# Kernel optimization log

Hardware: AMD Instinct MI355X
Metric: run time of the kernel (lower is better)

The kernel has to match this reference:

```python
import jax, jax.numpy as jnp
import numpy as np

H, T, D = 16, 2048, 1024
DH = D // H  # 64


def setup_inputs() -> dict:
    key = jax.random.key(0)
    ks = jax.random.split(key, 6)
    state = jax.random.normal(ks[0], (H, DH, DH), jnp.float32) * 0.02  # per-head recurrent state
    x = jax.random.normal(ks[1], (T, D), jnp.float32)
    done = jax.random.uniform(ks[2], (T,)) < (4.0 / T)  # sparse episode-reset flags (bool)
    w_qkv = jax.random.normal(ks[3], (D, 3 * D), jnp.float32) / np.sqrt(D)
    b_qkv = jnp.zeros((3 * D,), jnp.float32)
    w_out = jax.random.normal(ks[4], (D, D), jnp.float32) / np.sqrt(D)
    b_out = jnp.zeros((D,), jnp.float32)
    return {"state": state, "x": x, "done": done, "w_qkv": w_qkv,
            "b_qkv": b_qkv, "w_out": w_out, "b_out": b_out}


def _mha_forward(state, x, done, w_qkv, b_qkv, w_out, b_out):
    # qkv projection; einops 'T (QKV H Dh) -> QKV H T Dh'
    qkv = (x @ w_qkv + b_qkv).reshape(T, 3, H, DH).transpose(1, 2, 0, 3)
    q, k, v = qkv[0], qkv[1], qkv[2]  # each (H, T, Dh)

    cum = jnp.cumsum(done.astype(jnp.int32))  # inclusive cumsum, as in done.cumsum()
    before_first = cum == 0            # tokens before first reset (attend to carried state)
    after_last = cum == cum[-1]        # tokens after last reset (feed new state)
    done_any = cum[-1] > 0

    # make_attn_mask(done): causal AND no reset index i with s < i <= t.
    # The scanned mask equals: causal & (cum[t] == cum[s]) (same-segment).
    t_idx = jnp.arange(T)
    mask = (t_idx[:, None] >= t_idx[None, :]) & (cum[:, None] == cum[None, :])  # (T, T)

    attn = jnp.where(mask[None], jnp.einsum('htd,hsd->hts', q, k), 0.0)  # mask * (q @ k.T)
    q_bef = q * before_first[None, :, None]
    out = jnp.einsum('hts,hsd->htd', attn, v) + jnp.einsum('htd,hde->hte', q_bef, state)

    k_aft = k * after_last[None, :, None]
    v_aft = v * after_last[None, :, None]
    s_new = jnp.einsum('htd,hte->hde', k_aft, v_aft)  # k_aft.T @ v_aft per head
    new_state = jnp.where(done_any, s_new, state + s_new)

    # 'H T Dh -> T (H Dh)' then output projection
    x_out = out.transpose(1, 0, 2).reshape(T, D) @ w_out + b_out
    return new_state, x_out


def reference(state, x, done, w_qkv, b_qkv, w_out, b_out):
    return _mha_forward(state, x, done, w_qkv, b_qkv, w_out, b_out)
```

## Files before the change

### kernel.cpp

```cpp
#include <hip/hip_runtime.h>

#define TT 2048
#define DD 1024
#define HH 16
#define DH 64
#define QKV_N 3072
#define QKW 2048

typedef __attribute__((ext_vector_type(8))) short bf16x8;
typedef __attribute__((ext_vector_type(4))) short short4v;
typedef __attribute__((ext_vector_type(4))) float f32x4;

__device__ inline short f2bf(float f) {
    union { float f; unsigned u; } v; v.f = f;
    unsigned r = v.u + 0x7fff + ((v.u >> 16) & 1);
    return (short)(r >> 16);
}

__device__ inline f32x4 mfma16(bf16x8 a, bf16x8 b, f32x4 c) {
    return __builtin_amdgcn_mfma_f32_16x16x32_bf16(a, b, c, 0, 0, 0);
}

__device__ __forceinline__ void gload16(const void* g, void* l) {
    __builtin_amdgcn_global_load_lds(
        (const __attribute__((address_space(1))) unsigned int*)g,
        (__attribute__((address_space(3))) unsigned int*)l, 16, 0, 0);
}

__global__ __launch_bounds__(256) void scan_kernel(const int* __restrict__ done,
                                                   int* __restrict__ seg,
                                                   int* __restrict__ totalp,
                                                   int* __restrict__ aux) {
    __shared__ int part[256];
    __shared__ int excl[256];
    __shared__ int segl[2048];
    __shared__ int tot;
    int tid = threadIdx.x;
    int base = tid * 8;
    int local[8];
    int run = 0;
#pragma unroll
    for (int i = 0; i < 8; ++i) { run += (done[base + i] != 0) ? 1 : 0; local[i] = run; }
    part[tid] = run;
    __syncthreads();
    if (tid < 64) {
        int p4[4];
#pragma unroll
        for (int i = 0; i < 4; ++i) p4[i] = part[tid * 4 + i];
        int s = p4[0] + p4[1] + p4[2] + p4[3];
        int v = s;
#pragma unroll
        for (int off = 1; off < 64; off <<= 1) {
            int u = __shfl_up(v, off);
            if (tid >= off) v += u;
        }
        int ex = v - s;
#pragma unroll
        for (int i = 0; i < 4; ++i) { excl[tid * 4 + i] = ex; ex += p4[i]; }
        if (tid == 63) { totalp[0] = v; tot = v; }
    }
    __syncthreads();
    int off = excl[tid];
#pragma unroll
    for (int i = 0; i < 8; ++i) {
        int sv = off + local[i];
        seg[base + i] = sv;
        segl[base + i] = sv;
    }
    __syncthreads();
    if (tid < 33) {
        int target = (tid < 32) ? segl[tid * 64] : tot;
        int lo = 0, hi = 2047;
        while (lo < hi) { int mid = (lo + hi) >> 1; if (segl[mid] >= target) hi = mid; else lo = mid + 1; }
        aux[tid] = lo >> 6;
    }
}

__device__ void transpose_tile(const float* __restrict__ in, short* __restrict__ out,
                               int R, int C, int r0, int c0, float (*tile)[65]) {
    int tid = threadIdx.x;
#pragma unroll
    for (int p = 0; p < 4; ++p) {
        int ch = tid + p * 256;
        int r = ch >> 4, c4 = (ch & 15) * 4;
        float4 v = *(const float4*)&in[(size_t)(r0 + r) * C + c0 + c4];
        tile[r][c4] = v.x; tile[r][c4 + 1] = v.y; tile[r][c4 + 2] = v.z; tile[r][c4 + 3] = v.w;
    }
    __syncthreads();
#pragma unroll
    for (int p = 0; p < 2; ++p) {
        int ch = tid + p * 256;
        int c = ch >> 3, r8 = (ch & 7) * 8;
        short tmp[8];
#pragma unroll
        for (int i = 0; i < 8; ++i) tmp[i] = f2bf(tile[r8 + i][c]);
        *(float4*)&out[(size_t)(c0 + c) * R + r0 + r8] = *(float4*)tmp;
    }
}

__global__ __launch_bounds__(256) void prep_kernel(const float* __restrict__ x,
                                                   const float* __restrict__ w_qkv,
                                                   const float* __restrict__ w_out,
                                                   const float* __restrict__ state,
                                                   const int* __restrict__ totalp,
                                                   short* __restrict__ x_bf,
                                                   short* __restrict__ wqT,
                                                   short* __restrict__ woT,
                                                   short* __restrict__ stT,
                                                   float* __restrict__ stout) {
    __shared__ float tile[64][65];
    int b = blockIdx.x;
    if (b < 1024) {
        int i = (b * 256 + threadIdx.x) * 8;
        float4 a = *(const float4*)&x[i];
        float4 c = *(const float4*)&x[i + 4];
        short tmp[8] = {f2bf(a.x), f2bf(a.y), f2bf(a.z), f2bf(a.w),
                        f2bf(c.x), f2bf(c.y), f2bf(c.z), f2bf(c.w)};
        *(float4*)&x_bf[i] = *(float4*)tmp;
    } else if (b < 1792) {
        int bb = b - 1024;
        transpose_tile(w_qkv, wqT, DD, QKV_N, (bb & 15) * 64, (bb >> 4) * 64, tile);
    } else if (b < 2048) {
        int bb = b - 1792;
        transpose_tile(w_out, woT, DD, DD, (bb & 15) * 64, (bb >> 4) * 64, tile);
    } else if (b < 2064) {
        int h = b - 2048;
        transpose_tile(state + (size_t)h * 4096, stT + (size_t)h * 4096, DH, DH, 0, 0, tile);
    } else {
        int f = ((b - 2064) * 256 + threadIdx.x) * 4;
        bool done_any = totalp[0] > 0;
        float4 v = done_any ? make_float4(0.f, 0.f, 0.f, 0.f) : *(const float4*)&state[f];
        *(float4*)&stout[f] = v;
    }
}

__global__ __launch_bounds__(256) void gemm_qkv(const short* __restrict__ A,
                                                const short* __restrict__ BT,
                                                const float* __restrict__ bias,
                                                short* __restrict__ qk,
                                                short* __restrict__ vt) {
    __shared__ short As[128 * 32];
    __shared__ short Bs[128 * 32];
    const int K = DD, N = QKV_N;
    int tid = threadIdx.x;
    int wave = tid >> 6, lane = tid & 63;
    int quad = lane >> 4, l15 = lane & 15;
    int m0 = blockIdx.x * 128, n0 = blockIdx.y * 128;
    int wr = (wave >> 1) * 64, wc = (wave & 1) * 64;

    int srow = wave * 16 + (lane >> 2);
    int scol = (lane & 3) * 8;
    const short* Ag = A + (size_t)(m0 + srow) * K + scol;
    const short* Bg = BT + (size_t)(n0 + srow) * K + scol;
    short* As0 = &As[(wave * 16) * 32];
    short* As1 = &As[(64 + wave * 16) * 32];
    short* Bs0 = &Bs[(wave * 16) * 32];
    short* Bs1 = &Bs[(64 + wave * 16) * 32];

    f32x4 acc[4][4] = {};
    for (int k0 = 0; k0 < K; k0 += 32) {
        __syncthreads();
        gload16(Ag + k0, As0);
        gload16(Ag + (size_t)64 * K + k0, As1);
        gload16(Bg + k0, Bs0);
        gload16(Bg + (size_t)64 * K + k0, Bs1);
        __syncthreads();
        bf16x8 af[4], bfr[4];
#pragma unroll
        for (int i = 0; i < 4; ++i) {
            af[i]  = *(const bf16x8*)&As[(wr + i * 16 + l15) * 32 + quad * 8];
            bfr[i] = *(const bf16x8*)&Bs[(wc + i * 16 + l15) * 32 + quad * 8];
        }
#pragma unroll
        for (int i = 0; i < 4; ++i)
#pragma unroll
            for (int j = 0; j < 4; ++j)
                acc[i][j] = mfma16(af[i], bfr[j], acc[i][j]);
    }

    if (n0 < 2048) {
#pragma unroll
        for (int i = 0; i < 4; ++i)
#pragma unroll
            for (int j = 0; j < 4; ++j)
#pragma unroll
                for (int r = 0; r < 4; ++r) {
                    int row = m0 + wr + i * 16 + quad * 4 + r;
                    int col = n0 + wc + j * 16 + l15;
                    qk[(size_t)row * QKW + col] = f2bf(acc[i][j][r] + bias[col]);
                }
    } else {
#pragma unroll
        for (int j = 0; j < 4; ++j) {
            int col = n0 + wc + j * 16 + l15;
            float bv = bias[col];
            int eg = col - 2048;
            int hh = eg >> 6, e = eg & 63;
#pragma unroll
            for (int i = 0; i < 4; ++i) {
                int tb = m0 + wr + i * 16 + quad * 4;
                short4v pk;
#pragma unroll
                for (int r = 0; r < 4; ++r) pk[r] = f2bf(acc[i][j][r] + bv);
                *(short4v*)&vt[(size_t)hh * (DH * TT) + (size_t)e * TT + tb] = pk;
            }
        }
    }
}

__global__ __launch_bounds__(256) void attn_mfma(const short* __restrict__ qk,
                                                 const short* __restrict__ vt,
                                                 const short* __restrict__ stT,
                                                 const int* __restrict__ seg,
                                                 const int* __restrict__ aux,
                                                 short* __restrict__ outb) {
    __shared__ short Ss_lo[64 * 32];
    __shared__ short Ss_hi[64 * 32];

    int h = blockIdx.x, tt = blockIdx.y;
    int t0 = tt * 64;
    int tid = threadIdx.x, wave = tid >> 6, lane = tid & 63;
    int quad = lane >> 4, l15 = lane & 15;
    int myt = wave * 16;

    const short* qrow = qk + (size_t)(t0 + myt + l15) * QKW + h * DH + quad * 8;
    bf16x8 qf0 = *(const bf16x8*)qrow;
    bf16x8 qf1 = *(const bf16x8*)(qrow + 32);

    int tlane = t0 + myt + l15;
    int seg_lane = seg[tlane];
    int segt_r[4];
#pragma unroll
    for (int r = 0; r < 4; ++r) segt_r[r] = seg[t0 + myt + quad * 4 + r];

    f32x4 accT[4] = {};
    if (seg[t0] == 0) {
        const short* sb = stT + (size_t)h * 4096;
#pragma unroll
        for (int j = 0; j < 4; ++j) {
            const short* srow = sb + (j * 16 + l15) * 64 + quad * 8;
            bf16x8 a0 = *(const bf16x8*)srow;
            bf16x8 a1 = *(const bf16x8*)(srow + 32);
            accT[j] = mfma16(a0, qf0, accT[j]);
            accT[j] = mfma16(a1, qf1, accT[j]);
        }
        if (seg_lane != 0) {
#pragma unroll
            for (int j = 0; j < 4; ++j)
#pragma unroll
                for (int r = 0; r < 4; ++r) accT[j][r] = 0.f;
        }
    }

    short* ss_lo = &Ss_lo[myt * 32];
    short* ss_hi = &Ss_hi[myt * 32];
    const short* kbase = qk + 1024 + h * DH;
    const short* vbase = vt + (size_t)h * (DH * TT);

    int st0 = aux[tt];
    for (int st = st0; st <= tt; ++st) {
        int s0 = st * 64;
        f32x4 sacc[4] = {};
#pragma unroll
        for (int j = 0; j < 4; ++j) {
            const short* krow = kbase + (size_t)(s0 + j * 16 + l15) * QKW + quad * 8;
            bf16x8 b0 = *(const bf16x8*)krow;
            bf16x8 b1 = *(const bf16x8*)(krow + 32);
            sacc[j] = mfma16(qf0, b0, sacc[j]);
            sacc[j] = mfma16(qf1, b1, sacc[j]);
        }
        bool last = (st == tt);
#pragma unroll
        for (int j = 0; j < 4; ++j) {
            int sgl = s0 + j * 16 + l15;
            int seg_s = seg[sgl];
#pragma unroll
            for (int r = 0; r < 4; ++r) {
                bool ok = (seg_s == segt_r[r]);
                if (last) ok = ok && (sgl <= t0 + myt + quad * 4 + r);
                short v = ok ? f2bf(sacc[j][r]) : (short)0;
                int row = quad * 4 + r;
                if (j < 2) ss_lo[row * 32 + j * 16 + l15] = v;
                else       ss_hi[row * 32 + (j - 2) * 16 + l15] = v;
            }
        }
        bf16x8 sf0 = *(const bf16x8*)&ss_lo[l15 * 32 + quad * 8];
        bf16x8 sf1 = *(const bf16x8*)&ss_hi[l15 * 32 + quad * 8];
#pragma unroll
        for (int j = 0; j < 4; ++j) {
            const short* vrow = vbase + (size_t)(j * 16 + l15) * TT + s0 + quad * 8;
            bf16x8 a0 = *(const bf16x8*)vrow;
            bf16x8 a1 = *(const bf16x8*)(vrow + 32);
            accT[j] = mfma16(a0, sf0, accT[j]);
            accT[j] = mfma16(a1, sf1, accT[j]);
        }
    }

#pragma unroll
    for (int j = 0; j < 4; ++j) {
        short4v pk;
#pragma unroll
        for (int r = 0; r < 4; ++r) pk[r] = f2bf(accT[j][r]);
        *(short4v*)&outb[(size_t)tlane * DD + h * DH + j * 16 + quad * 4] = pk;
    }
}

__global__ __launch_bounds__(256) void state_mfma(const short* __restrict__ qk,
                                                  const short* __restrict__ vt,
                                                  const int* __restrict__ seg,
                                                  const int* __restrict__ totalp,
                                                  const int* __restrict__ aux,
                                                  float* __restrict__ out) {
    __shared__ short Kt_lo[64 * 32];
    __shared__ short Kt_hi[64 * 32];
    int h = blockIdx.x, ct = blockIdx.y;
    if (ct < aux[32]) return;
    int t0 = ct * 64;
    int total = totalp[0];
    int tid = threadIdx.x, wave = tid >> 6, lane = tid & 63;
    int quad = lane >> 4, l15 = lane & 15;
    int myd = wave * 16;

    {
        bool keep = (seg[t0 + lane] == total);
        const short* src = qk + (size_t)(t0 + lane) * QKW + 1024 + h * DH + myd;
        union { float4 f; short s[8]; } u0, u1;
        u0.f = keep ? *(const float4*)src : make_float4(0.f, 0.f, 0.f, 0.f);
        u1.f = keep ? *(const float4*)(src + 8) : make_float4(0.f, 0.f, 0.f, 0.f);
        short* dst = (lane < 32) ? &Kt_lo[lane] : &Kt_hi[lane - 32];
#pragma unroll
        for (int i = 0; i < 8; ++i) {
            dst[(myd + i) * 32] = u0.s[i];
            dst[(myd + 8 + i) * 32] = u1.s[i];
        }
    }
    bf16x8 a0 = *(const bf16x8*)&Kt_lo[(myd + l15) * 32 + quad * 8];
    bf16x8 a1 = *(const bf16x8*)&Kt_hi[(myd + l15) * 32 + quad * 8];

    const short* vbase = vt + (size_t)h * (DH * TT);
    f32x4 acc[4] = {};
#pragma unroll
    for (int j = 0; j < 4; ++j) {
        const short* vrow = vbase + (size_t)(j * 16 + l15) * TT + t0 + quad * 8;
        bf16x8 b0 = *(const bf16x8*)vrow;
        bf16x8 b1 = *(const bf16x8*)(vrow + 32);
        acc[j] = mfma16(a0, b0, acc[j]);
        acc[j] = mfma16(a1, b1, acc[j]);
    }
    float* oh = out + (size_t)h * 4096;
#pragma unroll
    for (int j = 0; j < 4; ++j)
#pragma unroll
        for (int r = 0; r < 4; ++r)
            atomicAdd(&oh[(myd + quad * 4 + r) * DH + j * 16 + l15], acc[j][r]);
}

__global__ __launch_bounds__(256) void gemm_out(const short* __restrict__ A,
                                                const short* __restrict__ BT,
                                                const float* __restrict__ bias,
                                                float* __restrict__ Cout,
                                                int M, int N, int K) {
    __shared__ short As[128 * 32];
    __shared__ short Bs[128 * 32];
    int tid = threadIdx.x;
    int wave = tid >> 6, lane = tid & 63;
    int quad = lane >> 4, l15 = lane & 15;
    int m0 = blockIdx.x * 128, n0 = blockIdx.y * 128;
    int wr = (wave >> 1) * 64, wc = (wave & 1) * 64;

    int srow = wave * 16 + (lane >> 2);
    int scol = (lane & 3) * 8;
    const short* Ag = A + (size_t)(m0 + srow) * K + scol;
    const short* Bg = BT + (size_t)(n0 + srow) * K + scol;
    short* As0 = &As[(wave * 16) * 32];
    short* As1 = &As[(64 + wave * 16) * 32];
    short* Bs0 = &Bs[(wave * 16) * 32];
    short* Bs1 = &Bs[(64 + wave * 16) * 32];

    f32x4 acc[4][4] = {};
    for (int k0 = 0; k0 < K; k0 += 32) {
        __syncthreads();
        gload16(Ag + k0, As0);
        gload16(Ag + (size_t)64 * K + k0, As1);
        gload16(Bg + k0, Bs0);
        gload16(Bg + (size_t)64 * K + k0, Bs1);
        __syncthreads();
        bf16x8 af[4], bfr[4];
#pragma unroll
        for (int i = 0; i < 4; ++i) {
            af[i]  = *(const bf16x8*)&As[(wr + i * 16 + l15) * 32 + quad * 8];
            bfr[i] = *(const bf16x8*)&Bs[(wc + i * 16 + l15) * 32 + quad * 8];
        }
#pragma unroll
        for (int i = 0; i < 4; ++i)
#pragma unroll
            for (int j = 0; j < 4; ++j)
                acc[i][j] = mfma16(af[i], bfr[j], acc[i][j]);
    }
#pragma unroll
    for (int i = 0; i < 4; ++i)
#pragma unroll
        for (int j = 0; j < 4; ++j)
#pragma unroll
            for (int r = 0; r < 4; ++r) {
                int row = m0 + wr + i * 16 + quad * 4 + r;
                int col = n0 + wc + j * 16 + l15;
                Cout[(size_t)row * N + col] = acc[i][j][r] + bias[col];
            }
}

extern "C" void kernel_launch(void* const* d_in, const int* in_sizes, int n_in,
                              void* d_out, int out_size, void* d_ws, size_t ws_size,
                              hipStream_t stream) {
    const float* state = (const float*)d_in[0];
    const float* x     = (const float*)d_in[1];
    const int*   done  = (const int*)d_in[2];
    const float* w_qkv = (const float*)d_in[3];
    const float* b_qkv = (const float*)d_in[4];
    const float* w_out = (const float*)d_in[5];
    const float* b_out = (const float*)d_in[6];

    char* ws = (char*)d_ws;
    int*   seg    = (int*)ws;
    int*   totalp = (int*)(ws + 8192);
    int*   aux    = (int*)(ws + 8256);
    short* wqT    = (short*)(ws + 8448);
    short* woT    = (short*)(ws + 6299904);
    short* stT    = (short*)(ws + 8397056);
    short* qk     = (short*)(ws + 8528128);
    short* vt     = (short*)(ws + 16916736);
    short* xbf_outb = (short*)(ws + 21111040);

    float* new_state_out = (float*)d_out;
    float* x_out         = (float*)d_out + HH * DH * DH;

    scan_kernel<<<1, 256, 0, stream>>>(done, seg, totalp, aux);
    prep_kernel<<<2128, 256, 0, stream>>>(x, w_qkv, w_out, state, totalp,
                                          xbf_outb, wqT, woT, stT, new_state_out);

    gemm_qkv<<<dim3(TT / 128, QKV_N / 128), 256, 0, stream>>>(
        xbf_outb, wqT, b_qkv, qk, vt);

    attn_mfma<<<dim3(HH, TT / 64), 256, 0, stream>>>(qk, vt, stT, seg, aux, xbf_outb);

    state_mfma<<<dim3(HH, TT / 64), 256, 0, stream>>>(qk, vt, seg, totalp, aux,
                                                      new_state_out);

    gemm_out<<<dim3(TT / 128, DD / 128), 256, 0, stream>>>(
        xbf_outb, woT, b_out, x_out, TT, DD, DD);
}
```

Measured before the change: 183.0 us.

## Split attention key range across chunks, fuse scan into prep and state into attention

The standalone scan kernel is folded into an extra block of the prep kernel, and the done_any check for the state copy is recomputed locally from the done flags. The state-update kernel becomes a fifth z-slice of the attention launch. Attention for each query tile is split across up to four key-chunk groups of eight tiles, with partial fp32 results written to a workspace and summed by a new reduce kernel. K and V loads are hoisted ahead of the MFMAs in each key-tile iteration. This aims to cut launch count and the serial load imbalance of long segments, at the cost of extra partial-sum traffic and one more kernel launch.

```diff
diff --git a/kernel.cpp b/kernel.cpp
--- a/kernel.cpp
+++ b/kernel.cpp
@@ -27,55 +27,6 @@
         (__attribute__((address_space(3))) unsigned int*)l, 16, 0, 0);
 }
 
-__global__ __launch_bounds__(256) void scan_kernel(const int* __restrict__ done,
-                                                   int* __restrict__ seg,
-                                                   int* __restrict__ totalp,
-                                                   int* __restrict__ aux) {
-    __shared__ int part[256];
-    __shared__ int excl[256];
-    __shared__ int segl[2048];
-    __shared__ int tot;
-    int tid = threadIdx.x;
-    int base = tid * 8;
-    int local[8];
-    int run = 0;
-#pragma unroll
-    for (int i = 0; i < 8; ++i) { run += (done[base + i] != 0) ? 1 : 0; local[i] = run; }
-    part[tid] = run;
-    __syncthreads();
-    if (tid < 64) {
-        int p4[4];
-#pragma unroll
-        for (int i = 0; i < 4; ++i) p4[i] = part[tid * 4 + i];
-        int s = p4[0] + p4[1] + p4[2] + p4[3];
-        int v = s;
-#pragma unroll
-        for (int off = 1; off < 64; off <<= 1) {
-            int u = __shfl_up(v, off);
-            if (tid >= off) v += u;
-        }
-        int ex = v - s;
-#pragma unroll
-        for (int i = 0; i < 4; ++i) { excl[tid * 4 + i] = ex; ex += p4[i]; }
-        if (tid == 63) { totalp[0] = v; tot = v; }
-    }
-    __syncthreads();
-    int off = excl[tid];
-#pragma unroll
-    for (int i = 0; i < 8; ++i) {
-        int sv = off + local[i];
-        seg[base + i] = sv;
-        segl[base + i] = sv;
-    }
-    __syncthreads();
-    if (tid < 33) {
-        int target = (tid < 32) ? segl[tid * 64] : tot;
-        int lo = 0, hi = 2047;
-        while (lo < hi) { int mid = (lo + hi) >> 1; if (segl[mid] >= target) hi = mid; else lo = mid + 1; }
-        aux[tid] = lo >> 6;
-    }
-}
-
 __device__ void transpose_tile(const float* __restrict__ in, short* __restrict__ out,
                                int R, int C, int r0, int c0, float (*tile)[65]) {
     int tid = threadIdx.x;
@@ -102,16 +53,21 @@
                                                    const float* __restrict__ w_qkv,
                                                    const float* __restrict__ w_out,
                                                    const float* __restrict__ state,
-                                                   const int* __restrict__ totalp,
+                                                   const int* __restrict__ done,
                                                    short* __restrict__ x_bf,
                                                    short* __restrict__ wqT,
                                                    short* __restrict__ woT,
                                                    short* __restrict__ stT,
-                                                   float* __restrict__ stout) {
+                                                   float* __restrict__ stout,
+                                                   int* __restrict__ seg,
+                                                   int* __restrict__ totalp,
+                                                   int* __restrict__ aux) {
     __shared__ float tile[64][65];
+    __shared__ int scanbuf[2048 + 512 + 1];
     int b = blockIdx.x;
+    int tid = threadIdx.x;
     if (b < 1024) {
-        int i = (b * 256 + threadIdx.x) * 8;
+        int i = (b * 256 + tid) * 8;
         float4 a = *(const float4*)&x[i];
         float4 c = *(const float4*)&x[i + 4];
         short tmp[8] = {f2bf(a.x), f2bf(a.y), f2bf(a.z), f2bf(a.w),
@@ -126,11 +82,60 @@
     } else if (b < 2064) {
         int h = b - 2048;
         transpose_tile(state + (size_t)h * 4096, stT + (size_t)h * 4096, DH, DH, 0, 0, tile);
+    } else if (b < 2128) {
+        __shared__ int anyf;
+        if (tid == 0) anyf = 0;
+        __syncthreads();
+        int acc = 0;
+#pragma unroll
+        for (int i = 0; i < 8; ++i) acc |= done[tid * 8 + i];
+        if (acc) anyf = 1;
+        __syncthreads();
+        int f = ((b - 2064) * 256 + tid) * 4;
+        float4 v = anyf ? make_float4(0.f, 0.f, 0.f, 0.f) : *(const float4*)&state[f];
+        *(float4*)&stout[f] = v;
     } else {
-        int f = ((b - 2064) * 256 + threadIdx.x) * 4;
-        bool done_any = totalp[0] > 0;
-        float4 v = done_any ? make_float4(0.f, 0.f, 0.f, 0.f) : *(const float4*)&state[f];
-        *(float4*)&stout[f] = v;
+        int* segl = scanbuf;
+        int* part = scanbuf + 2048;
+        int* excl = scanbuf + 2304;
+        int base = tid * 8;
+        int local[8];
+        int run = 0;
+#pragma unroll
+        for (int i = 0; i < 8; ++i) { run += (done[base + i] != 0) ? 1 : 0; local[i] = run; }
+        part[tid] = run;
+        __syncthreads();
+        if (tid < 64) {
+            int p4[4];
+#pragma unroll
+            for (int i = 0; i < 4; ++i) p4[i] = part[tid * 4 + i];
+            int s = p4[0] + p4[1] + p4[2] + p4[3];
+            int v = s;
+#pragma unroll
+            for (int off = 1; off < 64; off <<= 1) {
+                int u = __shfl_up(v, off);
+                if (tid >= off) v += u;
+            }
+            int ex = v - s;
+#pragma unroll
+            for (int i = 0; i < 4; ++i) { excl[tid * 4 + i] = ex; ex += p4[i]; }
+            if (tid == 63) { totalp[0] = v; scanbuf[2560] = v; }
+        }
+        __syncthreads();
+        int off = excl[tid];
+#pragma unroll
+        for (int i = 0; i < 8; ++i) {
+            int sv = off + local[i];
+            seg[base + i] = sv;
+            segl[base + i] = sv;
+        }
+        __syncthreads();
+        if (tid < 33) {
+            int target = (tid < 32) ? segl[tid * 64] : scanbuf[2560];
+            int lo = 0, hi = 2047;
+            while (lo < hi) { int mid = (lo + hi) >> 1; if (segl[mid] >= target) hi = mid; else lo = mid + 1; }
+            aux[tid] = lo >> 6;
+        }
     }
 }
 
@@ -141,7 +146,7 @@
                                                 short* __restrict__ vt) {
     __shared__ short As[128 * 32];
     __shared__ short Bs[128 * 32];
-    const int K = DD, N = QKV_N;
+    const int K = DD;
     int tid = threadIdx.x;
     int wave = tid >> 6, lane = tid & 63;
     int quad = lane >> 4, l15 = lane & 15;
@@ -212,16 +217,64 @@
                                                  const short* __restrict__ vt,
                                                  const short* __restrict__ stT,
                                                  const int* __restrict__ seg,
+                                                 const int* __restrict__ totalp,
                                                  const int* __restrict__ aux,
-                                                 short* __restrict__ outb) {
+                                                 short* __restrict__ outb,
+                                                 float* __restrict__ part,
+                                                 float* __restrict__ nsout) {
     __shared__ short Ss_lo[64 * 32];
     __shared__ short Ss_hi[64 * 32];
 
-    int h = blockIdx.x, tt = blockIdx.y;
+    int h = blockIdx.x, tt = blockIdx.y, sc = blockIdx.z;
     int t0 = tt * 64;
     int tid = threadIdx.x, wave = tid >> 6, lane = tid & 63;
     int quad = lane >> 4, l15 = lane & 15;
     int myt = wave * 16;
+    const short* vbase = vt + (size_t)h * (DH * TT);
+
+    if (sc == 4) {
+        if (tt < aux[32]) return;
+        int total = totalp[0];
+        int myd = myt;
+        {
+            bool keep = (seg[t0 + lane] == total);
+            const short* src = qk + (size_t)(t0 + lane) * QKW + 1024 + h * DH + myd;
+            union { float4 f; short s[8]; } u0, u1;
+            u0.f = keep ? *(const float4*)src : make_float4(0.f, 0.f, 0.f, 0.f);
+            u1.f = keep ? *(const float4*)(src + 8) : make_float4(0.f, 0.f, 0.f, 0.f);
+            short* dst = (lane < 32) ? &Ss_lo[lane] : &Ss_hi[lane - 32];
+#pragma unroll
+            for (int i = 0; i < 8; ++i) {
+                dst[(myd + i) * 32] = u0.s[i];
+                dst[(myd + 8 + i) * 32] = u1.s[i];
+            }
+        }
+        bf16x8 a0 = *(const bf16x8*)&Ss_lo[(myd + l15) * 32 + quad * 8];
+        bf16x8 a1 = *(const bf16x8*)&Ss_hi[(myd + l15) * 32 + quad * 8];
+        f32x4 acc[4] = {};
+#pragma unroll
+        for (int j = 0; j < 4; ++j) {
+            const short* vrow = vbase + (size_t)(j * 16 + l15) * TT + t0 + quad * 8;
+            bf16x8 b0 = *(const bf16x8*)vrow;
+            bf16x8 b1 = *(const bf16x8*)(vrow + 32);
+            acc[j] = mfma16(a0, b0, acc[j]);
+            acc[j] = mfma16(a1, b1, acc[j]);
+        }
+        float* oh = nsout + (size_t)h * 4096;
+#pragma unroll
+        for (int j = 0; j < 4; ++j)
+#pragma unroll
+            for (int r = 0; r < 4; ++r)
+                atomicAdd(&oh[(myd + quad * 4 + r) * DH + j * 16 + l15], acc[j][r]);
+        return;
+    }
+
+    int st0 = aux[tt];
+    int sc_lo = st0 >> 3, sc_hi = tt >> 3;
+    if (sc < sc_lo || sc > sc_hi) return;
+    bool direct = (sc_lo == sc_hi);
+    int st_lo = (st0 > sc * 8) ? st0 : sc * 8;
+    int st_hi = (tt < sc * 8 + 7) ? tt : sc * 8 + 7;
 
     const short* qrow = qk + (size_t)(t0 + myt + l15) * QKW + h * DH + quad * 8;
     bf16x8 qf0 = *(const bf16x8*)qrow;
@@ -234,7 +287,7 @@
     for (int r = 0; r < 4; ++r) segt_r[r] = seg[t0 + myt + quad * 4 + r];
 
     f32x4 accT[4] = {};
-    if (seg[t0] == 0) {
+    if (sc == sc_lo && seg[t0] == 0) {
         const short* sb = stT + (size_t)h * 4096;
 #pragma unroll
         for (int j = 0; j < 4; ++j) {
@@ -255,28 +308,39 @@
     short* ss_lo = &Ss_lo[myt * 32];
     short* ss_hi = &Ss_hi[myt * 32];
     const short* kbase = qk + 1024 + h * DH;
-    const short* vbase = vt + (size_t)h * (DH * TT);
-
-    int st0 = aux[tt];
-    for (int st = st0; st <= tt; ++st) {
+
+    for (int st = st_lo; st <= st_hi; ++st) {
         int s0 = st * 64;
+        int segv[4];
+#pragma unroll
+        for (int j = 0; j < 4; ++j) segv[j] = seg[s0 + j * 16 + l15];
+        bf16x8 kb0[4], kb1[4];
+#pragma unroll
+        for (int j = 0; j < 4; ++j) {
+            const short* krow = kbase + (size_t)(s0 + j * 16 + l15) * QKW + quad * 8;
+            kb0[j] = *(const bf16x8*)krow;
+            kb1[j] = *(const bf16x8*)(krow + 32);
+        }
+        bf16x8 va0[4], va1[4];
+#pragma unroll
+        for (int j = 0; j < 4; ++j) {
+            const short* vrow = vbase + (size_t)(j * 16 + l15) * TT + s0 + quad * 8;
+            va0[j] = *(const bf16x8*)vrow;
+            va1[j] = *(const bf16x8*)(vrow + 32);
+        }
         f32x4 sacc[4] = {};
 #pragma unroll
         for (int j = 0; j < 4; ++j) {
-            const short* krow = kbase + (size_t)(s0 + j * 16 + l15) * QKW + quad * 8;
-            bf16x8 b0 = *(const bf16x8*)krow;
-            bf16x8 b1 = *(const bf16x8*)(krow + 32);
-            sacc[j] = mfma16(qf0, b0, sacc[j]);
-            sacc[j] = mfma16(qf1, b1, sacc[j]);
+            sacc[j] = mfma16(qf0, kb0[j], sacc[j]);
+            sacc[j] = mfma16(qf1, kb1[j], sacc[j]);
         }
         bool last = (st == tt);
 #pragma unroll
         for (int j = 0; j < 4; ++j) {
             int sgl = s0 + j * 16 + l15;
-            int seg_s = seg[sgl];
 #pragma unroll
             for (int r = 0; r < 4; ++r) {
-                bool ok = (seg_s == segt_r[r]);
+                bool ok = (segv[j] == segt_r[r]);
                 if (last) ok = ok && (sgl <= t0 + myt + quad * 4 + r);
                 short v = ok ? f2bf(sacc[j][r]) : (short)0;
                 int row = quad * 4 + r;
@@ -288,71 +352,49 @@
         bf16x8 sf1 = *(const bf16x8*)&ss_hi[l15 * 32 + quad * 8];
 #pragma unroll
         for (int j = 0; j < 4; ++j) {
-            const short* vrow = vbase + (size_t)(j * 16 + l15) * TT + s0 + quad * 8;
-            bf16x8 a0 = *(const bf16x8*)vrow;
-            bf16x8 a1 = *(const bf16x8*)(vrow + 32);
-            accT[j] = mfma16(a0, sf0, accT[j]);
-            accT[j] = mfma16(a1, sf1, accT[j]);
-        }
-    }
-
-#pragma unroll
-    for (int j = 0; j < 4; ++j) {
+            accT[j] = mfma16(va0[j], sf0, accT[j]);
+            accT[j] = mfma16(va1[j], sf1, accT[j]);
+        }
+    }
+
+    if (direct) {
+#pragma unroll
+        for (int j = 0; j < 4; ++j) {
+            short4v pk;
+#pragma unroll
+            for (int r = 0; r < 4; ++r) pk[r] = f2bf(accT[j][r]);
+            *(short4v*)&outb[(size_t)tlane * DD + h * DH + j * 16 + quad * 4] = pk;
+        }
+    } else {
+        float* pb = part + (((size_t)(h * 32 + tt) * 4 + sc) * 4096);
+#pragma unroll
+        for (int j = 0; j < 4; ++j)
+            *(f32x4*)&pb[(myt + l15) * 64 + j * 16 + quad * 4] = accT[j];
+    }
+}
+
+__global__ __launch_bounds__(256) void attn_reduce(const float* __restrict__ part,
+                                                   const int* __restrict__ aux,
+                                                   short* __restrict__ outb) {
+    int h = blockIdx.x, tt = blockIdx.y;
+    int sc_lo = aux[tt] >> 3, sc_hi = tt >> 3;
+    if (sc_lo == sc_hi) return;
+    int t0 = tt * 64;
+    int tid = threadIdx.x;
+    int tl16 = tid >> 4, e4 = (tid & 15) * 4;
+    const float* pb = part + ((size_t)(h * 32 + tt) * 4) * 4096;
+#pragma unroll
+    for (int p = 0; p < 4; ++p) {
+        int tl = p * 16 + tl16;
+        float4 acc = make_float4(0.f, 0.f, 0.f, 0.f);
+        for (int sc = sc_lo; sc <= sc_hi; ++sc) {
+            float4 v = *(const float4*)&pb[sc * 4096 + tl * 64 + e4];
+            acc.x += v.x; acc.y += v.y; acc.z += v.z; acc.w += v.w;
+        }
         short4v pk;
-#pragma unroll
-        for (int r = 0; r < 4; ++r) pk[r] = f2bf(accT[j][r]);
-        *(short4v*)&outb[(size_t)tlane * DD + h * DH + j * 16 + quad * 4] = pk;
-    }
-}
-
-__global__ __launch_bounds__(256) void state_mfma(const short* __restrict__ qk,
-                                                  const short* __restrict__ vt,
-                                                  const int* __restrict__ seg,
-                                                  const int* __restrict__ totalp,
-                                                  const int* __restrict__ aux,
-                                                  float* __restrict__ out) {
-    __shared__ short Kt_lo[64 * 32];
-    __shared__ short Kt_hi[64 * 32];
-    int h = blockIdx.x, ct = blockIdx.y;
-    if (ct < aux[32]) return;
-    int t0 = ct * 64;
-    int total = totalp[0];
-    int tid = threadIdx.x, wave = tid >> 6, lane = tid & 63;
-    int quad = lane >> 4, l15 = lane & 15;
-    int myd = wave * 16;
-
-    {
-        bool keep = (seg[t0 + lane] == total);
-        const short* src = qk + (size_t)(t0 + lane) * QKW + 1024 + h * DH + myd;
-        union { float4 f; short s[8]; } u0, u1;
-        u0.f = keep ? *(const float4*)src : make_float4(0.f, 0.f, 0.f, 0.f);
-        u1.f = keep ? *(const float4*)(src + 8) : make_float4(0.f, 0.f, 0.f, 0.f);
-        short* dst = (lane < 32) ? &Kt_lo[lane] : &Kt_hi[lane - 32];
-#pragma unroll
-        for (int i = 0; i < 8; ++i) {
-            dst[(myd + i) * 32] = u0.s[i];
-            dst[(myd + 8 + i) * 32] = u1.s[i];
-        }
-    }
-    bf16x8 a0 = *(const bf16x8*)&Kt_lo[(myd + l15) * 32 + quad * 8];
-    bf16x8 a1 = *(const bf16x8*)&Kt_hi[(myd + l15) * 32 + quad * 8];
-
-    const short* vbase = vt + (size_t)h * (DH * TT);
-    f32x4 acc[4] = {};
-#pragma unroll
-    for (int j = 0; j < 4; ++j) {
-        const short* vrow = vbase + (size_t)(j * 16 + l15) * TT + t0 + quad * 8;
-        bf16x8 b0 = *(const bf16x8*)vrow;
-        bf16x8 b1 = *(const bf16x8*)(vrow + 32);
-        acc[j] = mfma16(a0, b0, acc[j]);
-        acc[j] = mfma16(a1, b1, acc[j]);
-    }
-    float* oh = out + (size_t)h * 4096;
-#pragma unroll
-    for (int j = 0; j < 4; ++j)
-#pragma unroll
-        for (int r = 0; r < 4; ++r)
-            atomicAdd(&oh[(myd + quad * 4 + r) * DH + j * 16 + l15], acc[j][r]);
+        pk[0] = f2bf(acc.x); pk[1] = f2bf(acc.y); pk[2] = f2bf(acc.z); pk[3] = f2bf(acc.w);
+        *(short4v*)&outb[(size_t)(t0 + tl) * DD + h * DH + e4] = pk;
+    }
 }
 
 __global__ __launch_bounds__(256) void gemm_out(const short* __restrict__ A,
@@ -430,21 +472,22 @@
     short* qk     = (short*)(ws + 8528128);
     short* vt     = (short*)(ws + 16916736);
     short* xbf_outb = (short*)(ws + 21111040);
+    float* part   = (float*)(ws + 25305344);
 
     float* new_state_out = (float*)d_out;
     float* x_out         = (float*)d_out + HH * DH * DH;
 
-    scan_kernel<<<1, 256, 0, stream>>>(done, seg, totalp, aux);
-    prep_kernel<<<2128, 256, 0, stream>>>(x, w_qkv, w_out, state, totalp,
-                                          xbf_outb, wqT, woT, stT, new_state_out);
+    prep_kernel<<<2129, 256, 0, stream>>>(x, w_qkv, w_out, state, done,
+                                          xbf_outb, wqT, woT, stT,
+                                          new_state_out, seg, totalp, aux);
 
     gemm_qkv<<<dim3(TT / 128, QKV_N / 128), 256, 0, stream>>>(
         xbf_outb, wqT, b_qkv, qk, vt);
 
-    attn_mfma<<<dim3(HH, TT / 64), 256, 0, stream>>>(qk, vt, stT, seg, aux, xbf_outb);
-
-    state_mfma<<<dim3(HH, TT / 64), 256, 0, stream>>>(qk, vt, seg, totalp, aux,
-                                                      new_state_out);
+    attn_mfma<<<dim3(HH, TT / 64, 5), 256, 0, stream>>>(
+        qk, vt, stT, seg, totalp, aux, xbf_outb, part, new_state_out);
+
+    attn_reduce<<<dim3(HH, TT / 64), 256, 0, stream>>>(part, aux, xbf_outb);
 
     gemm_out<<<dim3(TT / 128, DD / 128), 256, 0, stream>>>(
         xbf_outb, woT, b_out, x_out, TT, DD, DD);
```

After: 180.3 us. Within noise of the previous version (-1.4%).
